# Optimization experiments

Measured on AMD Instinct MI355X. Metric: run time of the kernel, lower is better.

## Reference

```python
import jax, jax.numpy as jnp
import numpy as np

B, T, D_IN, H, D_OUT = 4096, 512, 8, 50, 1

def setup_inputs() -> dict:
    key = jax.random.key(0)
    ks = jax.random.split(key, 7)
    s_ih = 1.0 / np.sqrt(H)
    return {
        "x": jax.random.normal(ks[0], (B, T, D_IN), dtype=jnp.float32),
        # torch nn.RNN params: weight_ih_l0 [H, D_IN], weight_hh_l0 [H, H], biases [H]
        "W_ih": jax.random.uniform(ks[1], (H, D_IN), minval=-s_ih, maxval=s_ih, dtype=jnp.float32),
        "W_hh": jax.random.uniform(ks[2], (H, H), minval=-s_ih, maxval=s_ih, dtype=jnp.float32),
        "b_ih": jax.random.uniform(ks[3], (H,), minval=-s_ih, maxval=s_ih, dtype=jnp.float32),
        "b_hh": jax.random.uniform(ks[4], (H,), minval=-s_ih, maxval=s_ih, dtype=jnp.float32),
        # fc: Linear(H, D_OUT)
        "fc_W": jax.random.uniform(ks[5], (D_OUT, H), minval=-s_ih, maxval=s_ih, dtype=jnp.float32),
        "fc_b": jax.random.uniform(ks[6], (D_OUT,), minval=-s_ih, maxval=s_ih, dtype=jnp.float32),
    }

def reference(x, W_ih, W_hh, b_ih, b_hh, fc_W, fc_b):
    # Vanilla RNN: h_t = tanh(x_t @ W_ih^T + b_ih + h_{t-1} @ W_hh^T + b_hh)
    # Precompute input projections for all timesteps (one big GEMM),
    # then scan the recurrence over time. Only the last hidden state is
    # needed because the module reads out[:, -1, :].
    xW = jnp.einsum('btd,hd->bth', x, W_ih) + (b_ih + b_hh)  # [B, T, H]
    xW_t = jnp.swapaxes(xW, 0, 1)  # [T, B, H] for scan over time

    def step(h, xw_t):
        h_new = jnp.tanh(xw_t + h @ W_hh.T)
        return h_new, None

    h0 = jnp.zeros((x.shape[0], W_hh.shape[0]), dtype=x.dtype)
    h_last, _ = jax.lax.scan(step, h0, xW_t)
    # fc on last timestep hidden
    return h_last @ fc_W.T + fc_b  # [B, D_OUT]
```

## Files before the change

kernel.cpp:

```cpp
#include <hip/hip_runtime.h>

#define B_TOT 4096
#define T_LEN 512
#define DIN   8
#define H_DIM 50

typedef __attribute__((ext_vector_type(8))) short  short8;
typedef __attribute__((ext_vector_type(4))) float  floatx4;

__device__ __forceinline__ ushort f2bf_rne(float f) {
  uint u = __float_as_uint(f);
  u += 0x7FFFu + ((u >> 16) & 1u);
  return (ushort)(u >> 16);
}
__device__ __forceinline__ ushort f2bf_trunc(float f) {
  return (ushort)(__float_as_uint(f) >> 16);
}
__device__ __forceinline__ float bf2f(ushort b) {
  return __uint_as_float(((uint)b) << 16);
}
__device__ __forceinline__ float fast_tanh(float v) {
  float e = __expf(2.0f * v);
  return 1.0f - 2.0f * __builtin_amdgcn_rcpf(1.0f + e);
}

#define ROWS 72
#define REG  1152

__global__ __launch_bounds__(256) void rnn_fused(
    const float* __restrict__ x, const float* __restrict__ W_ih,
    const float* __restrict__ W_hh, const float* __restrict__ b_ih,
    const float* __restrict__ b_hh, const float* __restrict__ fc_W,
    const float* __restrict__ fc_b, float* __restrict__ out)
{
  __shared__ __align__(16) ushort lds[4 * REG];

  const int tid  = threadIdx.x;
  const int lane = tid & 63;
  const int wave = tid >> 6;
  const int col  = lane & 15;
  const int kg   = lane >> 4;
  const int b0   = blockIdx.x * 16;

  const int iGlob = wave * 16 + col;
  union U8 { ushort u[8]; short8 v; };
  U8 Bh0u, Bh1u, Bl0u, Bl1u;
#pragma unroll
  for (int hf = 0; hf < 2; ++hf) {
#pragma unroll
    for (int j = 0; j < 8; ++j) {
      int k = hf * 32 + kg * 8 + j;
      float w = 0.f;
      if (iGlob < H_DIM) {
        if (k < H_DIM)            w = W_hh[iGlob * H_DIM + k];
        else if (k < H_DIM + DIN) w = W_ih[iGlob * DIN + (k - H_DIM)];
      }
      ushort hi = f2bf_rne(w);
      ushort lo = f2bf_trunc(w - bf2f(hi));
      if (hf == 0) { Bh0u.u[j] = hi; Bl0u.u[j] = lo; }
      else         { Bh1u.u[j] = hi; Bl1u.u[j] = lo; }
    }
  }
  const short8 Bh0 = Bh0u.v, Bh1 = Bh1u.v, Bl0 = Bl0u.v, Bl1 = Bl1u.v;

  const float bv = (iGlob < H_DIM) ? (b_ih[iGlob] + b_hh[iGlob]) : 0.f;
  const floatx4 biasf = {bv, bv, bv, bv};

  for (int z = tid; z < 4 * REG; z += 256) lds[z] = 0;
  __syncthreads();

  const int xm = tid >> 3;
  const int xd = tid & 7;
  const float* xp = x + ((size_t)(b0 + ((tid < 128) ? xm : 0)) * T_LEN) * DIN + xd;
  float px1 = 0.f, px2 = 0.f, px3 = 0.f;
  if (tid < 128) {
    float x0 = xp[0];
    ushort xh = f2bf_rne(x0);
    lds[0 * REG + xm * ROWS + H_DIM + xd] = xh;
    lds[1 * REG + xm * ROWS + H_DIM + xd] = f2bf_trunc(x0 - bf2f(xh));
    px1 = xp[8]; px2 = xp[16]; px3 = xp[24];
  }
  __syncthreads();

  auto step = [&](int t, int offph, int offpl, int offqh, int offql) {
    const int rb = col * ROWS + kg * 8;
    short8 Ah0 = *(const short8*)(lds + offph + rb);
    short8 Ah1 = *(const short8*)(lds + offph + rb + 32);
    short8 Al0 = *(const short8*)(lds + offpl + rb);
    short8 Al1 = *(const short8*)(lds + offpl + rb + 32);

    floatx4 acc = biasf;
    acc = __builtin_amdgcn_mfma_f32_16x16x32_bf16(Ah0, Bh0, acc, 0, 0, 0);
    acc = __builtin_amdgcn_mfma_f32_16x16x32_bf16(Ah1, Bh1, acc, 0, 0, 0);
    acc = __builtin_amdgcn_mfma_f32_16x16x32_bf16(Al0, Bh0, acc, 0, 0, 0);
    acc = __builtin_amdgcn_mfma_f32_16x16x32_bf16(Al1, Bh1, acc, 0, 0, 0);
    floatx4 accB = {0.f, 0.f, 0.f, 0.f};
    accB = __builtin_amdgcn_mfma_f32_16x16x32_bf16(Ah0, Bl0, accB, 0, 0, 0);
    accB = __builtin_amdgcn_mfma_f32_16x16x32_bf16(Ah1, Bl1, accB, 0, 0, 0);

    if (iGlob < H_DIM) {
#pragma unroll
      for (int r = 0; r < 4; ++r) {
        float v  = acc[r] + accB[r];
        float th = fast_tanh(v);
        ushort hi = f2bf_rne(th);
        ushort lo = f2bf_trunc(th - bf2f(hi));
        int m = kg * 4 + r;
        lds[offqh + m * ROWS + iGlob] = hi;
        lds[offql + m * ROWS + iGlob] = lo;
      }
    }
    if (tid < 128) {
      ushort xh = f2bf_rne(px1);
      ushort xl = f2bf_trunc(px1 - bf2f(xh));
      lds[offqh + xm * ROWS + H_DIM + xd] = xh;
      lds[offql + xm * ROWS + H_DIM + xd] = xl;
      px1 = px2; px2 = px3;
      int tn = t + 4; if (tn > T_LEN - 1) tn = T_LEN - 1;
      px3 = xp[tn * 8];
    }
    __syncthreads();
  };

  for (int t = 0; t < T_LEN; t += 2) {
    step(t,     0 * REG, 1 * REG, 2 * REG, 3 * REG);
    step(t + 1, 2 * REG, 3 * REG, 0 * REG, 1 * REG);
  }

  if (tid < 64) {
    int m = tid >> 2, kq = tid & 3;
    float acc2 = 0.f;
    for (int k = kq; k < H_DIM; k += 4) {
      float hv = bf2f(lds[0 * REG + m * ROWS + k]) + bf2f(lds[1 * REG + m * ROWS + k]);
      acc2 += hv * fc_W[k];
    }
    acc2 += __shfl_xor(acc2, 1);
    acc2 += __shfl_xor(acc2, 2);
    if (kq == 0) out[b0 + m] = acc2 + fc_b[0];
  }
}

extern "C" void kernel_launch(void* const* d_in, const int* in_sizes, int n_in,
                              void* d_out, int out_size, void* d_ws, size_t ws_size,
                              hipStream_t stream) {
  const float* x    = (const float*)d_in[0];
  const float* W_ih = (const float*)d_in[1];
  const float* W_hh = (const float*)d_in[2];
  const float* b_ih = (const float*)d_in[3];
  const float* b_hh = (const float*)d_in[4];
  const float* fc_W = (const float*)d_in[5];
  const float* fc_b = (const float*)d_in[6];
  rnn_fused<<<dim3(B_TOT / 16), dim3(256), 0, stream>>>(
      x, W_ih, W_hh, b_ih, b_hh, fc_W, fc_b, (float*)d_out);
}
```

Baseline: 296.9 us.

## Collapse RNN block to a single wave to drop per-step barriers

Each block now runs one 64-lane wave instead of four. That wave computes all four 16-column output tiles of the hidden state with MFMA, holding every W_hh/W_ih tile in registers, and the per-timestep __syncthreads goes away because a single wave needs no cross-wave barrier. The aim is to remove barrier latency on the serial recurrence. In exchange each wave does four times the MFMA and tanh work per step, uses more registers, and gets only one wave per block for latency hiding. It also relies on in-wave LDS ordering without any explicit wait or fence.

```diff
diff --git a/kernel.cpp b/kernel.cpp
--- a/kernel.cpp
+++ b/kernel.cpp
@@ -27,7 +27,7 @@
 #define ROWS 72
 #define REG  1152
 
-__global__ __launch_bounds__(256) void rnn_fused(
+__global__ __launch_bounds__(64, 1) void rnn_fused(
     const float* __restrict__ x, const float* __restrict__ W_ih,
     const float* __restrict__ W_hh, const float* __restrict__ b_ih,
     const float* __restrict__ b_hh, const float* __restrict__ fc_W,
@@ -35,91 +35,116 @@
 {
   __shared__ __align__(16) ushort lds[4 * REG];
 
-  const int tid  = threadIdx.x;
-  const int lane = tid & 63;
-  const int wave = tid >> 6;
+  const int lane = threadIdx.x;
   const int col  = lane & 15;
   const int kg   = lane >> 4;
   const int b0   = blockIdx.x * 16;
 
-  const int iGlob = wave * 16 + col;
   union U8 { ushort u[8]; short8 v; };
-  U8 Bh0u, Bh1u, Bl0u, Bl1u;
+  short8 Bh[4][2], Bl[4][2];
+  floatx4 biasf[4];
 #pragma unroll
-  for (int hf = 0; hf < 2; ++hf) {
+  for (int a = 0; a < 4; ++a) {
+    const int n = a * 16 + col;
+    const bool live = (n < H_DIM);
 #pragma unroll
-    for (int j = 0; j < 8; ++j) {
-      int k = hf * 32 + kg * 8 + j;
-      float w = 0.f;
-      if (iGlob < H_DIM) {
-        if (k < H_DIM)            w = W_hh[iGlob * H_DIM + k];
-        else if (k < H_DIM + DIN) w = W_ih[iGlob * DIN + (k - H_DIM)];
+    for (int hf = 0; hf < 2; ++hf) {
+      U8 bh, bl;
+#pragma unroll
+      for (int j = 0; j < 8; ++j) {
+        int k = hf * 32 + kg * 8 + j;
+        float w = 0.f;
+        if (live) {
+          if (k < H_DIM)            w = W_hh[n * H_DIM + k];
+          else if (k < H_DIM + DIN) w = W_ih[n * DIN + (k - H_DIM)];
+        }
+        ushort hi = f2bf_rne(w);
+        bh.u[j] = hi;
+        bl.u[j] = f2bf_trunc(w - bf2f(hi));
       }
-      ushort hi = f2bf_rne(w);
-      ushort lo = f2bf_trunc(w - bf2f(hi));
-      if (hf == 0) { Bh0u.u[j] = hi; Bl0u.u[j] = lo; }
-      else         { Bh1u.u[j] = hi; Bl1u.u[j] = lo; }
+      Bh[a][hf] = bh.v;
+      Bl[a][hf] = bl.v;
     }
+    const float bv = live ? (b_ih[n] + b_hh[n]) : 0.f;
+    biasf[a] = {bv, bv, bv, bv};
   }
-  const short8 Bh0 = Bh0u.v, Bh1 = Bh1u.v, Bl0 = Bl0u.v, Bl1 = Bl1u.v;
 
-  const float bv = (iGlob < H_DIM) ? (b_ih[iGlob] + b_hh[iGlob]) : 0.f;
-  const floatx4 biasf = {bv, bv, bv, bv};
+  for (int z = lane; z < 4 * REG; z += 64) lds[z] = 0;
 
-  for (int z = tid; z < 4 * REG; z += 256) lds[z] = 0;
-  __syncthreads();
+  const int xm = lane >> 3;
+  const int xd = lane & 7;
+  const float* xpA = x + ((size_t)(b0 + xm)     * T_LEN) * DIN + xd;
+  const float* xpB = x + ((size_t)(b0 + 8 + xm) * T_LEN) * DIN + xd;
+  {
+    float xa = xpA[0], xb = xpB[0];
+    ushort ha = f2bf_rne(xa), hb2 = f2bf_rne(xb);
+    lds[0 * REG + xm * ROWS + H_DIM + xd]       = ha;
+    lds[1 * REG + xm * ROWS + H_DIM + xd]       = f2bf_trunc(xa - bf2f(ha));
+    lds[0 * REG + (8 + xm) * ROWS + H_DIM + xd] = hb2;
+    lds[1 * REG + (8 + xm) * ROWS + H_DIM + xd] = f2bf_trunc(xb - bf2f(hb2));
+  }
+  float pA0 = xpA[DIN], pA1 = xpA[2 * DIN];
+  float pB0 = xpB[DIN], pB1 = xpB[2 * DIN];
 
-  const int xm = tid >> 3;
-  const int xd = tid & 7;
-  const float* xp = x + ((size_t)(b0 + ((tid < 128) ? xm : 0)) * T_LEN) * DIN + xd;
-  float px1 = 0.f, px2 = 0.f, px3 = 0.f;
-  if (tid < 128) {
-    float x0 = xp[0];
-    ushort xh = f2bf_rne(x0);
-    lds[0 * REG + xm * ROWS + H_DIM + xd] = xh;
-    lds[1 * REG + xm * ROWS + H_DIM + xd] = f2bf_trunc(x0 - bf2f(xh));
-    px1 = xp[8]; px2 = xp[16]; px3 = xp[24];
-  }
-  __syncthreads();
+  auto step = [&](int t, int ph, int pl, int qh, int ql) {
+    const int rb = col * ROWS + kg * 8;
+    short8 Ah0 = *(const short8*)(lds + ph + rb);
+    short8 Ah1 = *(const short8*)(lds + ph + rb + 32);
+    short8 Al0 = *(const short8*)(lds + pl + rb);
+    short8 Al1 = *(const short8*)(lds + pl + rb + 32);
 
-  auto step = [&](int t, int offph, int offpl, int offqh, int offql) {
-    const int rb = col * ROWS + kg * 8;
-    short8 Ah0 = *(const short8*)(lds + offph + rb);
-    short8 Ah1 = *(const short8*)(lds + offph + rb + 32);
-    short8 Al0 = *(const short8*)(lds + offpl + rb);
-    short8 Al1 = *(const short8*)(lds + offpl + rb + 32);
+    floatx4 vsum[4];
+#pragma unroll
+    for (int a = 0; a < 4; ++a) {
+      floatx4 acc = biasf[a];
+      acc = __builtin_amdgcn_mfma_f32_16x16x32_bf16(Ah0, Bh[a][0], acc, 0, 0, 0);
+      acc = __builtin_amdgcn_mfma_f32_16x16x32_bf16(Ah1, Bh[a][1], acc, 0, 0, 0);
+      floatx4 acc2 = {0.f, 0.f, 0.f, 0.f};
+      acc2 = __builtin_amdgcn_mfma_f32_16x16x32_bf16(Al0, Bh[a][0], acc2, 0, 0, 0);
+      acc2 = __builtin_amdgcn_mfma_f32_16x16x32_bf16(Al1, Bh[a][1], acc2, 0, 0, 0);
+      floatx4 accB = {0.f, 0.f, 0.f, 0.f};
+      accB = __builtin_amdgcn_mfma_f32_16x16x32_bf16(Ah0, Bl[a][0], accB, 0, 0, 0);
+      accB = __builtin_amdgcn_mfma_f32_16x16x32_bf16(Ah1, Bl[a][1], accB, 0, 0, 0);
+      vsum[a] = acc + acc2 + accB;
+    }
 
-    floatx4 acc = biasf;
-    acc = __builtin_amdgcn_mfma_f32_16x16x32_bf16(Ah0, Bh0, acc, 0, 0, 0);
-    acc = __builtin_amdgcn_mfma_f32_16x16x32_bf16(Ah1, Bh1, acc, 0, 0, 0);
-    acc = __builtin_amdgcn_mfma_f32_16x16x32_bf16(Al0, Bh0, acc, 0, 0, 0);
-    acc = __builtin_amdgcn_mfma_f32_16x16x32_bf16(Al1, Bh1, acc, 0, 0, 0);
-    floatx4 accB = {0.f, 0.f, 0.f, 0.f};
-    accB = __builtin_amdgcn_mfma_f32_16x16x32_bf16(Ah0, Bl0, accB, 0, 0, 0);
-    accB = __builtin_amdgcn_mfma_f32_16x16x32_bf16(Ah1, Bl1, accB, 0, 0, 0);
-
-    if (iGlob < H_DIM) {
+#pragma unroll
+    for (int a = 0; a < 3; ++a) {
+      const int n = a * 16 + col;
 #pragma unroll
       for (int r = 0; r < 4; ++r) {
-        float v  = acc[r] + accB[r];
-        float th = fast_tanh(v);
+        float th = fast_tanh(vsum[a][r]);
         ushort hi = f2bf_rne(th);
         ushort lo = f2bf_trunc(th - bf2f(hi));
         int m = kg * 4 + r;
-        lds[offqh + m * ROWS + iGlob] = hi;
-        lds[offql + m * ROWS + iGlob] = lo;
+        lds[qh + m * ROWS + n] = hi;
+        lds[ql + m * ROWS + n] = lo;
       }
     }
-    if (tid < 128) {
-      ushort xh = f2bf_rne(px1);
-      ushort xl = f2bf_trunc(px1 - bf2f(xh));
-      lds[offqh + xm * ROWS + H_DIM + xd] = xh;
-      lds[offql + xm * ROWS + H_DIM + xd] = xl;
-      px1 = px2; px2 = px3;
-      int tn = t + 4; if (tn > T_LEN - 1) tn = T_LEN - 1;
-      px3 = xp[tn * 8];
+    if (col < 2) {
+      const int n = 48 + col;
+#pragma unroll
+      for (int r = 0; r < 4; ++r) {
+        float th = fast_tanh(vsum[3][r]);
+        ushort hi = f2bf_rne(th);
+        ushort lo = f2bf_trunc(th - bf2f(hi));
+        int m = kg * 4 + r;
+        lds[qh + m * ROWS + n] = hi;
+        lds[ql + m * ROWS + n] = lo;
+      }
     }
-    __syncthreads();
+
+    {
+      ushort ha = f2bf_rne(pA0), hb2 = f2bf_rne(pB0);
+      lds[qh + xm * ROWS + H_DIM + xd]       = ha;
+      lds[ql + xm * ROWS + H_DIM + xd]       = f2bf_trunc(pA0 - bf2f(ha));
+      lds[qh + (8 + xm) * ROWS + H_DIM + xd] = hb2;
+      lds[ql + (8 + xm) * ROWS + H_DIM + xd] = f2bf_trunc(pB0 - bf2f(hb2));
+      pA0 = pA1; pB0 = pB1;
+      int tn = t + 3; if (tn > T_LEN - 1) tn = T_LEN - 1;
+      pA1 = xpA[(size_t)tn * DIN];
+      pB1 = xpB[(size_t)tn * DIN];
+    }
   };
 
   for (int t = 0; t < T_LEN; t += 2) {
@@ -127,16 +152,16 @@
     step(t + 1, 2 * REG, 3 * REG, 0 * REG, 1 * REG);
   }
 
-  if (tid < 64) {
-    int m = tid >> 2, kq = tid & 3;
-    float acc2 = 0.f;
+  {
+    int m = lane >> 2, kq = lane & 3;
+    float accr = 0.f;
     for (int k = kq; k < H_DIM; k += 4) {
       float hv = bf2f(lds[0 * REG + m * ROWS + k]) + bf2f(lds[1 * REG + m * ROWS + k]);
-      acc2 += hv * fc_W[k];
+      accr += hv * fc_W[k];
     }
-    acc2 += __shfl_xor(acc2, 1);
-    acc2 += __shfl_xor(acc2, 2);
-    if (kq == 0) out[b0 + m] = acc2 + fc_b[0];
+    accr += __shfl_xor(accr, 1);
+    accr += __shfl_xor(accr, 2);
+    if (kq == 0) out[b0 + m] = accr + fc_b[0];
   }
 }
 
@@ -150,6 +175,6 @@
   const float* b_hh = (const float*)d_in[4];
   const float* fc_W = (const float*)d_in[5];
   const float* fc_b = (const float*)d_in[6];
-  rnn_fused<<<dim3(B_TOT / 16), dim3(256), 0, stream>>>(
+  rnn_fused<<<dim3(B_TOT / 16), dim3(64), 0, stream>>>(
       x, W_ih, W_hh, b_ih, b_hh, fc_W, fc_b, (float*)d_out);
 }
```

Measured after the change: 528.8 us. 1.78x slower.

## Interleave hi/lo bf16 halves in LDS and split MFMA chains into four accumulators

Applied to the files above, without the earlier changes.

The hidden state and input are now stored as packed hi/lo bf16 pairs in one 32-bit LDS word instead of two separate planes. The weight fragments are arranged to match, so each K=32 MFMA consumes hi and lo products together. The recurrence step now issues 8 MFMAs across four independent accumulators with dependency depth 2, instead of 6 MFMAs with a 4-deep chain. The write-back uses one 32-bit LDS store per element instead of two 16-bit stores. The cost is extra MFMA work per step, including a lo*lo term, in exchange for shorter serial latency on the critical path.

```diff
diff --git a/kernel.cpp b/kernel.cpp
--- a/kernel.cpp
+++ b/kernel.cpp
@@ -4,6 +4,11 @@
 #define T_LEN 512
 #define DIN   8
 #define H_DIM 50
+
+#define ROWS_U 136
+#define ROW_UI 68
+#define REG_US 2176
+#define REG_UI 1088
 
 typedef __attribute__((ext_vector_type(8))) short  short8;
 typedef __attribute__((ext_vector_type(4))) float  floatx4;
@@ -24,16 +29,14 @@
   return 1.0f - 2.0f * __builtin_amdgcn_rcpf(1.0f + e);
 }
 
-#define ROWS 72
-#define REG  1152
-
 __global__ __launch_bounds__(256) void rnn_fused(
     const float* __restrict__ x, const float* __restrict__ W_ih,
     const float* __restrict__ W_hh, const float* __restrict__ b_ih,
     const float* __restrict__ b_hh, const float* __restrict__ fc_W,
     const float* __restrict__ fc_b, float* __restrict__ out)
 {
-  __shared__ __align__(16) ushort lds[4 * REG];
+  __shared__ __align__(16) ushort lds[2 * REG_US];
+  uint* const lds32 = (uint*)lds;
 
   const int tid  = threadIdx.x;
   const int lane = tid & 63;
@@ -42,101 +45,107 @@
   const int kg   = lane >> 4;
   const int b0   = blockIdx.x * 16;
 
-  const int iGlob = wave * 16 + col;
+  const int nG = wave * 16 + col;
+  const bool live = (nG < H_DIM);
   union U8 { ushort u[8]; short8 v; };
-  U8 Bh0u, Bh1u, Bl0u, Bl1u;
+  short8 Bs[4], Bw[4];
 #pragma unroll
-  for (int hf = 0; hf < 2; ++hf) {
+  for (int c = 0; c < 4; ++c) {
+    U8 bs, bw;
 #pragma unroll
-    for (int j = 0; j < 8; ++j) {
-      int k = hf * 32 + kg * 8 + j;
+    for (int j2 = 0; j2 < 4; ++j2) {
+      const int p = c * 16 + kg * 4 + j2;
       float w = 0.f;
-      if (iGlob < H_DIM) {
-        if (k < H_DIM)            w = W_hh[iGlob * H_DIM + k];
-        else if (k < H_DIM + DIN) w = W_ih[iGlob * DIN + (k - H_DIM)];
+      if (live) {
+        if (p < H_DIM)            w = W_hh[nG * H_DIM + p];
+        else if (p < H_DIM + DIN) w = W_ih[nG * DIN + (p - H_DIM)];
       }
       ushort hi = f2bf_rne(w);
       ushort lo = f2bf_trunc(w - bf2f(hi));
-      if (hf == 0) { Bh0u.u[j] = hi; Bl0u.u[j] = lo; }
-      else         { Bh1u.u[j] = hi; Bl1u.u[j] = lo; }
+      bs.u[2 * j2]     = hi;  bs.u[2 * j2 + 1] = lo;
+      bw.u[2 * j2]     = lo;  bw.u[2 * j2 + 1] = hi;
     }
+    Bs[c] = bs.v;
+    Bw[c] = bw.v;
   }
-  const short8 Bh0 = Bh0u.v, Bh1 = Bh1u.v, Bl0 = Bl0u.v, Bl1 = Bl1u.v;
+  const float bv = live ? (b_ih[nG] + b_hh[nG]) : 0.f;
+  const floatx4 biasf = {bv, bv, bv, bv};
+  const floatx4 zf    = {0.f, 0.f, 0.f, 0.f};
 
-  const float bv = (iGlob < H_DIM) ? (b_ih[iGlob] + b_hh[iGlob]) : 0.f;
-  const floatx4 biasf = {bv, bv, bv, bv};
-
-  for (int z = tid; z < 4 * REG; z += 256) lds[z] = 0;
+  for (int z = tid; z < 2 * REG_UI; z += 256) lds32[z] = 0;
   __syncthreads();
 
   const int xm = tid >> 3;
   const int xd = tid & 7;
-  const float* xp = x + ((size_t)(b0 + ((tid < 128) ? xm : 0)) * T_LEN) * DIN + xd;
+  const bool xthr = (tid < 128);
+  const float* xp = x + ((size_t)(b0 + (xthr ? xm : 0)) * T_LEN) * DIN + xd;
   float px1 = 0.f, px2 = 0.f, px3 = 0.f;
-  if (tid < 128) {
+  if (xthr) {
     float x0 = xp[0];
-    ushort xh = f2bf_rne(x0);
-    lds[0 * REG + xm * ROWS + H_DIM + xd] = xh;
-    lds[1 * REG + xm * ROWS + H_DIM + xd] = f2bf_trunc(x0 - bf2f(xh));
+    ushort hi = f2bf_rne(x0);
+    ushort lo = f2bf_trunc(x0 - bf2f(hi));
+    lds32[xm * ROW_UI + H_DIM + xd] = (uint)hi | ((uint)lo << 16);
     px1 = xp[8]; px2 = xp[16]; px3 = xp[24];
   }
   __syncthreads();
 
-  auto step = [&](int t, int offph, int offpl, int offqh, int offql) {
-    const int rb = col * ROWS + kg * 8;
-    short8 Ah0 = *(const short8*)(lds + offph + rb);
-    short8 Ah1 = *(const short8*)(lds + offph + rb + 32);
-    short8 Al0 = *(const short8*)(lds + offpl + rb);
-    short8 Al1 = *(const short8*)(lds + offpl + rb + 32);
+  auto step = [&](int t, const ushort* lp, uint* q32) {
+    const int rb = col * ROWS_U + kg * 8;
+    short8 A0 = *(const short8*)(lp + rb);
+    short8 A1 = *(const short8*)(lp + rb + 32);
+    short8 A2 = *(const short8*)(lp + rb + 64);
+    short8 A3 = *(const short8*)(lp + rb + 96);
 
-    floatx4 acc = biasf;
-    acc = __builtin_amdgcn_mfma_f32_16x16x32_bf16(Ah0, Bh0, acc, 0, 0, 0);
-    acc = __builtin_amdgcn_mfma_f32_16x16x32_bf16(Ah1, Bh1, acc, 0, 0, 0);
-    acc = __builtin_amdgcn_mfma_f32_16x16x32_bf16(Al0, Bh0, acc, 0, 0, 0);
-    acc = __builtin_amdgcn_mfma_f32_16x16x32_bf16(Al1, Bh1, acc, 0, 0, 0);
-    floatx4 accB = {0.f, 0.f, 0.f, 0.f};
-    accB = __builtin_amdgcn_mfma_f32_16x16x32_bf16(Ah0, Bl0, accB, 0, 0, 0);
-    accB = __builtin_amdgcn_mfma_f32_16x16x32_bf16(Ah1, Bl1, accB, 0, 0, 0);
+    floatx4 ch0 = biasf;
+    ch0 = __builtin_amdgcn_mfma_f32_16x16x32_bf16(A0, Bs[0], ch0, 0, 0, 0);
+    ch0 = __builtin_amdgcn_mfma_f32_16x16x32_bf16(A1, Bs[1], ch0, 0, 0, 0);
+    floatx4 ch1 = zf;
+    ch1 = __builtin_amdgcn_mfma_f32_16x16x32_bf16(A0, Bw[0], ch1, 0, 0, 0);
+    ch1 = __builtin_amdgcn_mfma_f32_16x16x32_bf16(A1, Bw[1], ch1, 0, 0, 0);
+    floatx4 ch2 = zf;
+    ch2 = __builtin_amdgcn_mfma_f32_16x16x32_bf16(A2, Bs[2], ch2, 0, 0, 0);
+    ch2 = __builtin_amdgcn_mfma_f32_16x16x32_bf16(A3, Bs[3], ch2, 0, 0, 0);
+    floatx4 ch3 = zf;
+    ch3 = __builtin_amdgcn_mfma_f32_16x16x32_bf16(A2, Bw[2], ch3, 0, 0, 0);
+    ch3 = __builtin_amdgcn_mfma_f32_16x16x32_bf16(A3, Bw[3], ch3, 0, 0, 0);
+    floatx4 vsum = (ch0 + ch1) + (ch2 + ch3);
 
-    if (iGlob < H_DIM) {
+    if (live) {
 #pragma unroll
       for (int r = 0; r < 4; ++r) {
-        float v  = acc[r] + accB[r];
-        float th = fast_tanh(v);
+        float th = fast_tanh(vsum[r]);
         ushort hi = f2bf_rne(th);
         ushort lo = f2bf_trunc(th - bf2f(hi));
-        int m = kg * 4 + r;
-        lds[offqh + m * ROWS + iGlob] = hi;
-        lds[offql + m * ROWS + iGlob] = lo;
+        q32[(kg * 4 + r) * ROW_UI + nG] = (uint)hi | ((uint)lo << 16);
       }
     }
-    if (tid < 128) {
-      ushort xh = f2bf_rne(px1);
-      ushort xl = f2bf_trunc(px1 - bf2f(xh));
-      lds[offqh + xm * ROWS + H_DIM + xd] = xh;
-      lds[offql + xm * ROWS + H_DIM + xd] = xl;
+    if (xthr) {
+      ushort hi = f2bf_rne(px1);
+      ushort lo = f2bf_trunc(px1 - bf2f(hi));
+      q32[xm * ROW_UI + H_DIM + xd] = (uint)hi | ((uint)lo << 16);
       px1 = px2; px2 = px3;
       int tn = t + 4; if (tn > T_LEN - 1) tn = T_LEN - 1;
-      px3 = xp[tn * 8];
+      px3 = xp[(size_t)tn * DIN];
     }
     __syncthreads();
   };
 
   for (int t = 0; t < T_LEN; t += 2) {
-    step(t,     0 * REG, 1 * REG, 2 * REG, 3 * REG);
-    step(t + 1, 2 * REG, 3 * REG, 0 * REG, 1 * REG);
+    step(t,     lds,          lds32 + REG_UI);
+    step(t + 1, lds + REG_US, lds32);
   }
 
   if (tid < 64) {
-    int m = tid >> 2, kq = tid & 3;
-    float acc2 = 0.f;
+    int m = lane >> 2, kq = lane & 3;
+    float accr = 0.f;
     for (int k = kq; k < H_DIM; k += 4) {
-      float hv = bf2f(lds[0 * REG + m * ROWS + k]) + bf2f(lds[1 * REG + m * ROWS + k]);
-      acc2 += hv * fc_W[k];
+      uint pk = lds32[m * ROW_UI + k];
+      float hv = bf2f((ushort)(pk & 0xFFFFu)) + bf2f((ushort)(pk >> 16));
+      accr += hv * fc_W[k];
     }
-    acc2 += __shfl_xor(acc2, 1);
-    acc2 += __shfl_xor(acc2, 2);
-    if (kq == 0) out[b0 + m] = acc2 + fc_b[0];
+    accr += __shfl_xor(accr, 1);
+    accr += __shfl_xor(accr, 2);
+    if (kq == 0) out[b0 + m] = accr + fc_b[0];
   }
 }
 
```

New measurement: 321.3 us. +8.2%, slower.

## Run whole RNN recurrence in one wave with register-resident hidden state

Applied to the files above, without the earlier changes.

Replaces the 4-wave block that exchanged the hidden state through LDS with barriers every step by a single 64-lane wave per 16-batch tile. It computes all four 16-row output tiles itself, using the transposed MFMA form so the output accumulator layout can be repacked directly into the next step's B operand. Packing hi and lo bf16 parts into interleaved pairs folds the split-precision terms into the K dimension. This removes the per-step LDS round trip and __syncthreads, in exchange for four times more MFMA work per wave, fewer waves to hide latency, and heavy register use.

```diff
diff --git a/kernel.cpp b/kernel.cpp
--- a/kernel.cpp
+++ b/kernel.cpp
@@ -24,120 +24,134 @@
   return 1.0f - 2.0f * __builtin_amdgcn_rcpf(1.0f + e);
 }
 
-#define ROWS 72
-#define REG  1152
+__device__ __forceinline__ void packHL(float v, uint& rs, uint& rw) {
+  uint u  = __float_as_uint(v);
+  uint hi = (u + (0x7FFFu + ((u >> 16) & 1u))) >> 16;
+  uint hb = hi << 16;
+  float resid = v - __uint_as_float(hb);
+  uint lo = __float_as_uint(resid) >> 16;
+  rs = hi | (lo << 16);
+  rw = lo | hb;
+}
 
-__global__ __launch_bounds__(256) void rnn_fused(
+__global__ __launch_bounds__(64, 1) void rnn_fused(
     const float* __restrict__ x, const float* __restrict__ W_ih,
     const float* __restrict__ W_hh, const float* __restrict__ b_ih,
     const float* __restrict__ b_hh, const float* __restrict__ fc_W,
     const float* __restrict__ fc_b, float* __restrict__ out)
 {
-  __shared__ __align__(16) ushort lds[4 * REG];
-
-  const int tid  = threadIdx.x;
-  const int lane = tid & 63;
-  const int wave = tid >> 6;
+  const int lane = threadIdx.x;
   const int col  = lane & 15;
   const int kg   = lane >> 4;
   const int b0   = blockIdx.x * 16;
 
-  const int iGlob = wave * 16 + col;
-  union U8 { ushort u[8]; short8 v; };
-  U8 Bh0u, Bh1u, Bl0u, Bl1u;
+  union FU { uint u[4]; short8 v; };
+
+  short8 Aw[4][4];
 #pragma unroll
-  for (int hf = 0; hf < 2; ++hf) {
+  for (int mt = 0; mt < 4; ++mt) {
+    const int i = mt * 16 + col;
+    const bool ilive = (i < H_DIM);
 #pragma unroll
-    for (int j = 0; j < 8; ++j) {
-      int k = hf * 32 + kg * 8 + j;
-      float w = 0.f;
-      if (iGlob < H_DIM) {
-        if (k < H_DIM)            w = W_hh[iGlob * H_DIM + k];
-        else if (k < H_DIM + DIN) w = W_ih[iGlob * DIN + (k - H_DIM)];
+    for (int f = 0; f < 4; ++f) {
+      FU a;
+#pragma unroll
+      for (int j2 = 0; j2 < 4; ++j2) {
+        const int p = f * 16 + kg * 4 + j2;
+        float w = 0.f;
+        if (ilive) {
+          if (p < H_DIM)            w = W_hh[i * H_DIM + p];
+          else if (p < H_DIM + DIN) w = W_ih[i * DIN + (p - H_DIM)];
+        }
+        ushort hi = f2bf_rne(w);
+        ushort lo = f2bf_trunc(w - bf2f(hi));
+        a.u[j2] = (uint)hi | ((uint)lo << 16);
       }
-      ushort hi = f2bf_rne(w);
-      ushort lo = f2bf_trunc(w - bf2f(hi));
-      if (hf == 0) { Bh0u.u[j] = hi; Bl0u.u[j] = lo; }
-      else         { Bh1u.u[j] = hi; Bl1u.u[j] = lo; }
+      Aw[mt][f] = a.v;
     }
   }
-  const short8 Bh0 = Bh0u.v, Bh1 = Bh1u.v, Bl0 = Bl0u.v, Bl1 = Bl1u.v;
+  floatx4 biasv[4];
+#pragma unroll
+  for (int mt = 0; mt < 4; ++mt)
+#pragma unroll
+    for (int r = 0; r < 4; ++r) {
+      const int i = mt * 16 + kg * 4 + r;
+      biasv[mt][r] = (i < H_DIM) ? (b_ih[i] + b_hh[i]) : 0.f;
+    }
 
-  const float bv = (iGlob < H_DIM) ? (b_ih[iGlob] + b_hh[iGlob]) : 0.f;
-  const floatx4 biasf = {bv, bv, bv, bv};
+  const int dA = (kg == 0) ? 0 : (kg == 1) ? 2 : (kg == 2) ? 6 : 0;
+  const int dB = (kg == 1) ? 4 : dA;
+  const float* xrow = x + (size_t)(b0 + col) * T_LEN * DIN;
+  float2 qA0 = *(const float2*)(xrow + 0 * DIN + dA);
+  float2 qB0 = *(const float2*)(xrow + 0 * DIN + dB);
+  float2 qA1 = *(const float2*)(xrow + 1 * DIN + dA);
+  float2 qB1 = *(const float2*)(xrow + 1 * DIN + dB);
+  float2 qA2 = *(const float2*)(xrow + 2 * DIN + dA);
+  float2 qB2 = *(const float2*)(xrow + 2 * DIN + dB);
 
-  for (int z = tid; z < 4 * REG; z += 256) lds[z] = 0;
-  __syncthreads();
+  float th[4][4];
+#pragma unroll
+  for (int mt = 0; mt < 4; ++mt)
+#pragma unroll
+    for (int r = 0; r < 4; ++r) th[mt][r] = 0.f;
 
-  const int xm = tid >> 3;
-  const int xd = tid & 7;
-  const float* xp = x + ((size_t)(b0 + ((tid < 128) ? xm : 0)) * T_LEN) * DIN + xd;
-  float px1 = 0.f, px2 = 0.f, px3 = 0.f;
-  if (tid < 128) {
-    float x0 = xp[0];
-    ushort xh = f2bf_rne(x0);
-    lds[0 * REG + xm * ROWS + H_DIM + xd] = xh;
-    lds[1 * REG + xm * ROWS + H_DIM + xd] = f2bf_trunc(x0 - bf2f(xh));
-    px1 = xp[8]; px2 = xp[16]; px3 = xp[24];
-  }
-  __syncthreads();
+  for (int t = 0; t < T_LEN; ++t) {
+    FU bs[4], bw[4];
+#pragma unroll
+    for (int f = 0; f < 3; ++f)
+#pragma unroll
+      for (int p = 0; p < 4; ++p)
+        packHL(th[f][p], bs[f].u[p], bw[f].u[p]);
 
-  auto step = [&](int t, int offph, int offpl, int offqh, int offql) {
-    const int rb = col * ROWS + kg * 8;
-    short8 Ah0 = *(const short8*)(lds + offph + rb);
-    short8 Ah1 = *(const short8*)(lds + offph + rb + 32);
-    short8 Al0 = *(const short8*)(lds + offpl + rb);
-    short8 Al1 = *(const short8*)(lds + offpl + rb + 32);
+    float v3_0, v3_1, v3_2, v3_3;
+    if (kg == 0)      { v3_0 = th[3][0]; v3_1 = th[3][1]; v3_2 = qA0.x; v3_3 = qA0.y; }
+    else if (kg == 1) { v3_0 = qA0.x;    v3_1 = qA0.y;    v3_2 = qB0.x; v3_3 = qB0.y; }
+    else if (kg == 2) { v3_0 = qA0.x;    v3_1 = qA0.y;    v3_2 = 0.f;   v3_3 = 0.f; }
+    else              { v3_0 = 0.f;      v3_1 = 0.f;      v3_2 = 0.f;   v3_3 = 0.f; }
+    packHL(v3_0, bs[3].u[0], bw[3].u[0]);
+    packHL(v3_1, bs[3].u[1], bw[3].u[1]);
+    packHL(v3_2, bs[3].u[2], bw[3].u[2]);
+    packHL(v3_3, bs[3].u[3], bw[3].u[3]);
 
-    floatx4 acc = biasf;
-    acc = __builtin_amdgcn_mfma_f32_16x16x32_bf16(Ah0, Bh0, acc, 0, 0, 0);
-    acc = __builtin_amdgcn_mfma_f32_16x16x32_bf16(Ah1, Bh1, acc, 0, 0, 0);
-    acc = __builtin_amdgcn_mfma_f32_16x16x32_bf16(Al0, Bh0, acc, 0, 0, 0);
-    acc = __builtin_amdgcn_mfma_f32_16x16x32_bf16(Al1, Bh1, acc, 0, 0, 0);
-    floatx4 accB = {0.f, 0.f, 0.f, 0.f};
-    accB = __builtin_amdgcn_mfma_f32_16x16x32_bf16(Ah0, Bl0, accB, 0, 0, 0);
-    accB = __builtin_amdgcn_mfma_f32_16x16x32_bf16(Ah1, Bl1, accB, 0, 0, 0);
+    qA0 = qA1; qB0 = qB1; qA1 = qA2; qB1 = qB2;
+    {
+      int tn = t + 3; if (tn > T_LEN - 1) tn = T_LEN - 1;
+      qA2 = *(const float2*)(xrow + (size_t)tn * DIN + dA);
+      qB2 = *(const float2*)(xrow + (size_t)tn * DIN + dB);
+    }
 
-    if (iGlob < H_DIM) {
 #pragma unroll
-      for (int r = 0; r < 4; ++r) {
-        float v  = acc[r] + accB[r];
-        float th = fast_tanh(v);
-        ushort hi = f2bf_rne(th);
-        ushort lo = f2bf_trunc(th - bf2f(hi));
-        int m = kg * 4 + r;
-        lds[offqh + m * ROWS + iGlob] = hi;
-        lds[offql + m * ROWS + iGlob] = lo;
+    for (int mt = 0; mt < 4; ++mt) {
+      floatx4 aS = biasv[mt];
+      aS = __builtin_amdgcn_mfma_f32_16x16x32_bf16(Aw[mt][0], bs[0].v, aS, 0, 0, 0);
+      aS = __builtin_amdgcn_mfma_f32_16x16x32_bf16(Aw[mt][1], bs[1].v, aS, 0, 0, 0);
+      aS = __builtin_amdgcn_mfma_f32_16x16x32_bf16(Aw[mt][2], bs[2].v, aS, 0, 0, 0);
+      aS = __builtin_amdgcn_mfma_f32_16x16x32_bf16(Aw[mt][3], bs[3].v, aS, 0, 0, 0);
+      floatx4 aW = {0.f, 0.f, 0.f, 0.f};
+      aW = __builtin_amdgcn_mfma_f32_16x16x32_bf16(Aw[mt][0], bw[0].v, aW, 0, 0, 0);
+      aW = __builtin_amdgcn_mfma_f32_16x16x32_bf16(Aw[mt][1], bw[1].v, aW, 0, 0, 0);
+      aW = __builtin_amdgcn_mfma_f32_16x16x32_bf16(Aw[mt][2], bw[2].v, aW, 0, 0, 0);
+      aW = __builtin_amdgcn_mfma_f32_16x16x32_bf16(Aw[mt][3], bw[3].v, aW, 0, 0, 0);
+      floatx4 s = aS + aW;
+      th[mt][0] = fast_tanh(s[0]);
+      th[mt][1] = fast_tanh(s[1]);
+      if (mt < 3) {
+        th[mt][2] = fast_tanh(s[2]);
+        th[mt][3] = fast_tanh(s[3]);
       }
     }
-    if (tid < 128) {
-      ushort xh = f2bf_rne(px1);
-      ushort xl = f2bf_trunc(px1 - bf2f(xh));
-      lds[offqh + xm * ROWS + H_DIM + xd] = xh;
-      lds[offql + xm * ROWS + H_DIM + xd] = xl;
-      px1 = px2; px2 = px3;
-      int tn = t + 4; if (tn > T_LEN - 1) tn = T_LEN - 1;
-      px3 = xp[tn * 8];
-    }
-    __syncthreads();
-  };
-
-  for (int t = 0; t < T_LEN; t += 2) {
-    step(t,     0 * REG, 1 * REG, 2 * REG, 3 * REG);
-    step(t + 1, 2 * REG, 3 * REG, 0 * REG, 1 * REG);
   }
 
-  if (tid < 64) {
-    int m = tid >> 2, kq = tid & 3;
-    float acc2 = 0.f;
-    for (int k = kq; k < H_DIM; k += 4) {
-      float hv = bf2f(lds[0 * REG + m * ROWS + k]) + bf2f(lds[1 * REG + m * ROWS + k]);
-      acc2 += hv * fc_W[k];
-    }
-    acc2 += __shfl_xor(acc2, 1);
-    acc2 += __shfl_xor(acc2, 2);
-    if (kq == 0) out[b0 + m] = acc2 + fc_b[0];
-  }
+  float p = 0.f;
+#pragma unroll
+  for (int mt = 0; mt < 3; ++mt)
+#pragma unroll
+    for (int r = 0; r < 4; ++r)
+      p += th[mt][r] * fc_W[mt * 16 + kg * 4 + r];
+  if (kg == 0) p += th[3][0] * fc_W[48] + th[3][1] * fc_W[49];
+  p += __shfl_xor(p, 16);
+  p += __shfl_xor(p, 32);
+  if (kg == 0) out[b0 + col] = p + fc_b[0];
 }
 
 extern "C" void kernel_launch(void* const* d_in, const int* in_sizes, int n_in,
@@ -150,6 +164,6 @@
   const float* b_hh = (const float*)d_in[4];
   const float* fc_W = (const float*)d_in[5];
   const float* fc_b = (const float*)d_in[6];
-  rnn_fused<<<dim3(B_TOT / 16), dim3(256), 0, stream>>>(
+  rnn_fused<<<dim3(B_TOT / 16), dim3(64), 0, stream>>>(
       x, W_ih, W_hh, b_ih, b_hh, fc_W, fc_b, (float*)d_out);
 }
```

After: 438.8 us. +47.8%, slower.
